# Kernel optimization log

Measured on AMD Instinct MI355X. Metric: run time of the kernel, lower is better.

## Reference

```python
import jax, jax.numpy as jnp
import numpy as np

N_FFT = 1024
N_STAGES = 3
N_SUB = N_FFT >> N_STAGES      # 128-point base IDFT
N_CHUNKS = 1 << N_STAGES       # 8 chunks after partial bit-reversal


def _mod_seq(order):
    mset = [0]
    for o in range(order):
        step = 2 ** o
        mset = [v for x in mset for v in (x, x + step)]
    return mset


def _perm_matrix(N, order):
    m = np.zeros((N, N), dtype=np.float32)
    base = 2 ** order
    k = 0
    for p in _mod_seq(order):
        for j in range(N // base):
            m[j * base + p, k] = 1.0
            k += 1
    return m


PERM = jnp.asarray(_perm_matrix(N_FFT, N_STAGES))
_idft = np.fft.ifft(np.eye(N_SUB))
IDFT_R = jnp.asarray(_idft.real.astype(np.float32))
IDFT_I = jnp.asarray(_idft.imag.astype(np.float32))


def _twiddle(n_fft_stage):
    w = np.exp(2j * np.pi / n_fft_stage) ** np.arange(n_fft_stage // 2)  # inverse sign
    return (jnp.asarray(w.real.astype(np.float32)),
            jnp.asarray(w.imag.astype(np.float32)))


TWIDDLES = []
_stage_size = N_FFT // 2 ** (N_STAGES - 1)
for _ in range(N_STAGES):
    TWIDDLES.append(_twiddle(_stage_size))
    _stage_size *= 2


def _idft_apply(re, im):
    yr = re @ IDFT_R.T - im @ IDFT_I.T
    yi = re @ IDFT_I.T + im @ IDFT_R.T
    return yr, yi


def _ifft_forward(re, im):
    # partial bit-reversal permutation then chunk
    re_p = jnp.split(re @ PERM, N_CHUNKS, axis=-1)
    im_p = jnp.split(im @ PERM, N_CHUNKS, axis=-1)
    ev_r, ev_i, od_r, od_i = [], [], [], []
    for j in range(N_CHUNKS // 2):
        er, ei = _idft_apply(re_p[2 * j], im_p[2 * j])
        o_r, o_i = _idft_apply(re_p[2 * j + 1], im_p[2 * j + 1])
        ev_r.append(er); ev_i.append(ei); od_r.append(o_r); od_i.append(o_i)
    # butterfly twiddle stages
    for tr, ti in TWIDDLES:
        ner, nei, nor, noi = [], [], [], []
        for i in range(len(ev_r)):
            todd_r = tr * od_r[i] - ti * od_i[i]
            todd_i = tr * od_i[i] + ti * od_r[i]
            real = jnp.concatenate([ev_r[i] + todd_r, ev_r[i] - todd_r], axis=-1)
            imag = jnp.concatenate([ev_i[i] + todd_i, ev_i[i] - todd_i], axis=-1)
            if i % 2 == 0:
                ner.append(real); nei.append(imag)
            else:
                nor.append(real); noi.append(imag)
        ev_r, ev_i, od_r, od_i = ner, nei, nor, noi
    scale = 1.0 / (1 << N_STAGES)  # IFFTNormalizer
    return ev_r[0] * scale, ev_i[0] * scale


def setup_inputs() -> dict:
    key = jax.random.key(0)
    k1, k2 = jax.random.split(key)
    re = jax.random.normal(k1, (8, 4096, N_FFT), dtype=jnp.float32)
    im = jax.random.normal(k2, (8, 4096, N_FFT), dtype=jnp.float32)
    return {"re": re, "im": im}


def reference(re, im):
    return _ifft_forward(re, im)
```

## Files before the change

kernel.cpp:

```cpp
#include <hip/hip_runtime.h>

#define NFFT 1024
#define TWO_PI 6.28318530717958647692f

__device__ __forceinline__ int SW(int a) {
    return a ^ ((((a >> 5) ^ (a >> 8)) & 7) << 2);
}

__device__ __forceinline__ void bfly4(float& r0, float& i0, float& r1, float& i1,
                                      float& r2, float& i2, float& r3, float& i3) {
    float d0r = r0 + r2, d0i = i0 + i2;
    float d1r = r0 - r2, d1i = i0 - i2;
    float d2r = r1 + r3, d2i = i1 + i3;
    float sr  = r1 - r3, si  = i1 - i3;
    r0 = d0r + d2r; i0 = d0i + d2i;
    r2 = d0r - d2r; i2 = d0i - d2i;
    r1 = d1r - si;  i1 = d1i + sr;
    r3 = d1r + si;  i3 = d1i - sr;
}

__device__ __forceinline__ void twmul(float& x, float& y, float c, float s) {
    float t = x * c - y * s;
    y = x * s + y * c;
    x = t;
}

__global__ __launch_bounds__(64, 4) void ifft1024_kernel(
        const float* __restrict__ re, const float* __restrict__ im,
        float* __restrict__ out, size_t imoff) {
    __shared__ __align__(16) float lds[2048];
    const int u = threadIdx.x;
    const size_t rowb = (size_t)blockIdx.x * NFFT;

    float vr[4][4], vi[4][4];

#pragma unroll
    for (int b = 0; b < 4; ++b)
#pragma unroll
        for (int a = 0; a < 4; ++a) {
            int idx = u + 64 * a + 256 * b;
            vr[a][b] = re[rowb + idx];
            vi[a][b] = im[rowb + idx];
        }

#pragma unroll
    for (int a = 0; a < 4; ++a) {
        bfly4(vr[a][0], vi[a][0], vr[a][1], vi[a][1],
              vr[a][2], vi[a][2], vr[a][3], vi[a][3]);
        float ang = (TWO_PI / 1024.f) * (float)(u + 64 * a);
        float s1, c1; __sincosf(ang, &s1, &c1);
        float c2 = c1 * c1 - s1 * s1, s2 = 2.f * c1 * s1;
        float c3 = c2 * c1 - s2 * s1, s3 = c2 * s1 + s2 * c1;
        twmul(vr[a][1], vi[a][1], c1, s1);
        twmul(vr[a][2], vi[a][2], c2, s2);
        twmul(vr[a][3], vi[a][3], c3, s3);
    }

    {
        float ang = (TWO_PI / 256.f) * (float)u;
        float s1, c1; __sincosf(ang, &s1, &c1);
        float c2 = c1 * c1 - s1 * s1, s2 = 2.f * c1 * s1;
        float c3 = c2 * c1 - s2 * s1, s3 = c2 * s1 + s2 * c1;
#pragma unroll
        for (int b = 0; b < 4; ++b) {
            bfly4(vr[0][b], vi[0][b], vr[1][b], vi[1][b],
                  vr[2][b], vi[2][b], vr[3][b], vi[3][b]);
            twmul(vr[1][b], vi[1][b], c1, s1);
            twmul(vr[2][b], vi[2][b], c2, s2);
            twmul(vr[3][b], vi[3][b], c3, s3);
        }
    }

#pragma unroll
    for (int b = 0; b < 4; ++b) {
        *(float4*)&lds[SW(16 * u + 4 * b)] =
            make_float4(vr[0][b], vr[1][b], vr[2][b], vr[3][b]);
        *(float4*)&lds[SW(16 * u + 4 * b + 1024)] =
            make_float4(vi[0][b], vi[1][b], vi[2][b], vi[3][b]);
    }
    __syncthreads();
    {
        int lo = (u >> 2) + 16 * (u & 3);
#pragma unroll
        for (int b = 0; b < 4; ++b)
#pragma unroll
            for (int a = 0; a < 4; ++a) {
                int q = lo + 64 * a + 256 * b;
                vr[a][b] = lds[SW(q)];
                vi[a][b] = lds[SW(q + 1024)];
            }
    }

    const int w = u & 3;
#pragma unroll
    for (int a = 0; a < 4; ++a) {
        bfly4(vr[a][0], vi[a][0], vr[a][1], vi[a][1],
              vr[a][2], vi[a][2], vr[a][3], vi[a][3]);
        float ang = (TWO_PI / 64.f) * (float)(w + 4 * a);
        float s1, c1; __sincosf(ang, &s1, &c1);
        float c2 = c1 * c1 - s1 * s1, s2 = 2.f * c1 * s1;
        float c3 = c2 * c1 - s2 * s1, s3 = c2 * s1 + s2 * c1;
        twmul(vr[a][1], vi[a][1], c1, s1);
        twmul(vr[a][2], vi[a][2], c2, s2);
        twmul(vr[a][3], vi[a][3], c3, s3);
    }

    {
        float ang = (TWO_PI / 16.f) * (float)w;
        float s1, c1; __sincosf(ang, &s1, &c1);
        float c2 = c1 * c1 - s1 * s1, s2 = 2.f * c1 * s1;
        float c3 = c2 * c1 - s2 * s1, s3 = c2 * s1 + s2 * c1;
#pragma unroll
        for (int b = 0; b < 4; ++b) {
            bfly4(vr[0][b], vi[0][b], vr[1][b], vi[1][b],
                  vr[2][b], vi[2][b], vr[3][b], vi[3][b]);
            twmul(vr[1][b], vi[1][b], c1, s1);
            twmul(vr[2][b], vi[2][b], c2, s2);
            twmul(vr[3][b], vi[3][b], c3, s3);
        }
    }
    __syncthreads();

#pragma unroll
    for (int a = 0; a < 4; ++a) {
        *(float4*)&lds[SW(16 * u + 4 * a)] =
            make_float4(vr[a][0], vr[a][1], vr[a][2], vr[a][3]);
        *(float4*)&lds[SW(16 * u + 4 * a + 1024)] =
            make_float4(vi[a][0], vi[a][1], vi[a][2], vi[a][3]);
    }
    __syncthreads();
    {
        int lo = (u & 3) + 64 * (u >> 2);
#pragma unroll
        for (int c = 0; c < 4; ++c)
#pragma unroll
            for (int e = 0; e < 4; ++e) {
                int q = lo + 4 * c + 16 * e;
                vr[c][e] = lds[SW(q)];
                vi[c][e] = lds[SW(q + 1024)];
            }
    }

#pragma unroll
    for (int c = 0; c < 4; ++c)
        bfly4(vr[c][0], vi[c][0], vr[c][1], vi[c][1],
              vr[c][2], vi[c][2], vr[c][3], vi[c][3]);

    const float sc = 1.f / 1024.f;
    const int nbase = 16 * (u & 3) + 4 * ((u >> 2) & 3) + (u >> 4);
#pragma unroll
    for (int e = 0; e < 4; ++e)
#pragma unroll
        for (int c = 0; c < 4; ++c) {
            int n = nbase + 64 * c + 256 * e;
            out[rowb + n]         = vr[c][e] * sc;
            out[imoff + rowb + n] = vi[c][e] * sc;
        }
}

extern "C" void kernel_launch(void* const* d_in, const int* in_sizes, int n_in,
                              void* d_out, int out_size, void* d_ws, size_t ws_size,
                              hipStream_t stream) {
    const float* re = (const float*)d_in[0];
    const float* im = (const float*)d_in[1];
    float* out = (float*)d_out;
    const int rows = in_sizes[0] / NFFT;
    const size_t im_off = (size_t)in_sizes[0];

    hipLaunchKernelGGL(ifft1024_kernel, dim3(rows), dim3(64), 0, stream,
                       re, im, out, im_off);
}
```

Before: 434.5 us.

## Pack four rows per block, one wavefront each, and restructure FFT data flow

Each 256-thread block now handles four 1024-point rows, one per wavefront, with a private LDS slice and only block-level fences in place of __syncthreads. Inputs are read as float4, twiddles come from one sincos plus rotation recurrences, and the last radix-16 stage uses constant twiddles after a float4 LDS read. A simpler XOR swizzle replaces the old one. This aims to cut per-block overhead, barrier cost and transcendental work, but it relies on wavefront-synchronous LDS behaviour and adds some twiddle rounding error from the recurrence.

Measured after the change: 433.2 us. Within noise of the previous version (-0.3%).

```diff
diff --git a/kernel.cpp b/kernel.cpp
--- a/kernel.cpp
+++ b/kernel.cpp
@@ -2,10 +2,6 @@
 
 #define NFFT 1024
 #define TWO_PI 6.28318530717958647692f
-
-__device__ __forceinline__ int SW(int a) {
-    return a ^ ((((a >> 5) ^ (a >> 8)) & 7) << 2);
-}
 
 __device__ __forceinline__ void bfly4(float& r0, float& i0, float& r1, float& i1,
                                       float& r2, float& i2, float& r3, float& i3) {
@@ -25,136 +21,164 @@
     x = t;
 }
 
-__global__ __launch_bounds__(64, 4) void ifft1024_kernel(
+__global__ __launch_bounds__(256, 4) void ifft1024_kernel(
         const float* __restrict__ re, const float* __restrict__ im,
         float* __restrict__ out, size_t imoff) {
-    __shared__ __align__(16) float lds[2048];
-    const int u = threadIdx.x;
-    const size_t rowb = (size_t)blockIdx.x * NFFT;
+    __shared__ __align__(16) float lds_all[8192];
+    const int tid = threadIdx.x;
+    const int u   = tid & 63;
+    const int wv  = tid >> 6;
+    float* lds = lds_all + (wv << 11);
+
+    const size_t row  = (size_t)blockIdx.x * 4 + wv;
+    const size_t rowb = row * NFFT;
 
     float vr[4][4], vi[4][4];
-
 #pragma unroll
-    for (int b = 0; b < 4; ++b)
-#pragma unroll
-        for (int a = 0; a < 4; ++a) {
-            int idx = u + 64 * a + 256 * b;
-            vr[a][b] = re[rowb + idx];
-            vi[a][b] = im[rowb + idx];
-        }
-
-#pragma unroll
-    for (int a = 0; a < 4; ++a) {
-        bfly4(vr[a][0], vi[a][0], vr[a][1], vi[a][1],
-              vr[a][2], vi[a][2], vr[a][3], vi[a][3]);
-        float ang = (TWO_PI / 1024.f) * (float)(u + 64 * a);
-        float s1, c1; __sincosf(ang, &s1, &c1);
-        float c2 = c1 * c1 - s1 * s1, s2 = 2.f * c1 * s1;
-        float c3 = c2 * c1 - s2 * s1, s3 = c2 * s1 + s2 * c1;
-        twmul(vr[a][1], vi[a][1], c1, s1);
-        twmul(vr[a][2], vi[a][2], c2, s2);
-        twmul(vr[a][3], vi[a][3], c3, s3);
+    for (int b = 0; b < 4; ++b) {
+        float4 r4 = *(const float4*)(re + rowb + 4 * u + 256 * b);
+        float4 i4 = *(const float4*)(im + rowb + 4 * u + 256 * b);
+        vr[0][b] = r4.x; vr[1][b] = r4.y; vr[2][b] = r4.z; vr[3][b] = r4.w;
+        vi[0][b] = i4.x; vi[1][b] = i4.y; vi[2][b] = i4.z; vi[3][b] = i4.w;
     }
 
     {
-        float ang = (TWO_PI / 256.f) * (float)u;
-        float s1, c1; __sincosf(ang, &s1, &c1);
-        float c2 = c1 * c1 - s1 * s1, s2 = 2.f * c1 * s1;
-        float c3 = c2 * c1 - s2 * s1, s3 = c2 * s1 + s2 * c1;
+        float c1, s1;
+        __sincosf((TWO_PI / 256.f) * (float)u, &s1, &c1);
+        const float CS = 0.9999811752826011f;
+        const float SN = 0.0061358846491544753f;
 #pragma unroll
-        for (int b = 0; b < 4; ++b) {
-            bfly4(vr[0][b], vi[0][b], vr[1][b], vi[1][b],
-                  vr[2][b], vi[2][b], vr[3][b], vi[3][b]);
-            twmul(vr[1][b], vi[1][b], c1, s1);
-            twmul(vr[2][b], vi[2][b], c2, s2);
-            twmul(vr[3][b], vi[3][b], c3, s3);
+        for (int k = 0; k < 4; ++k) {
+            bfly4(vr[k][0], vi[k][0], vr[k][1], vi[k][1],
+                  vr[k][2], vi[k][2], vr[k][3], vi[k][3]);
+            float c2 = c1 * c1 - s1 * s1, s2 = 2.f * c1 * s1;
+            float c3 = c2 * c1 - s2 * s1, s3 = c2 * s1 + s2 * c1;
+            twmul(vr[k][1], vi[k][1], c1, s1);
+            twmul(vr[k][2], vi[k][2], c2, s2);
+            twmul(vr[k][3], vi[k][3], c3, s3);
+            float nc = c1 * CS - s1 * SN, ns = c1 * SN + s1 * CS;
+            c1 = nc; s1 = ns;
         }
     }
 
 #pragma unroll
     for (int b = 0; b < 4; ++b) {
-        *(float4*)&lds[SW(16 * u + 4 * b)] =
-            make_float4(vr[0][b], vr[1][b], vr[2][b], vr[3][b]);
-        *(float4*)&lds[SW(16 * u + 4 * b + 1024)] =
-            make_float4(vi[0][b], vi[1][b], vi[2][b], vi[3][b]);
+        int q = (4 * u + 256 * b) ^ ((b & 1) << 4);
+        *(float4*)&lds[q]        = make_float4(vr[0][b], vr[1][b], vr[2][b], vr[3][b]);
+        *(float4*)&lds[q + 1024] = make_float4(vi[0][b], vi[1][b], vi[2][b], vi[3][b]);
     }
-    __syncthreads();
+    __threadfence_block();
+
+    const int j = u & 15, h = u >> 4;
+    const int flip = (h & 1) << 4;
+    float wr[4][4], wi[4][4];
     {
-        int lo = (u >> 2) + 16 * (u & 3);
+        const int rb = j + 256 * h;
 #pragma unroll
-        for (int b = 0; b < 4; ++b)
+        for (int a = 0; a < 4; ++a)
 #pragma unroll
-            for (int a = 0; a < 4; ++a) {
-                int q = lo + 64 * a + 256 * b;
-                vr[a][b] = lds[SW(q)];
-                vi[a][b] = lds[SW(q + 1024)];
+            for (int c = 0; c < 4; ++c) {
+                int q = rb + ((16 * a) ^ flip) + 64 * c;
+                wr[a][c] = lds[q];
+                wi[a][c] = lds[q + 1024];
             }
     }
 
-    const int w = u & 3;
+    {
+        float cA, sA;
+        __sincosf((TWO_PI / 256.f) * (float)j, &sA, &cA);
+        const float CS8 = 0.9238795325112867f;
+        const float SN8 = 0.3826834323650898f;
 #pragma unroll
-    for (int a = 0; a < 4; ++a) {
-        bfly4(vr[a][0], vi[a][0], vr[a][1], vi[a][1],
-              vr[a][2], vi[a][2], vr[a][3], vi[a][3]);
-        float ang = (TWO_PI / 64.f) * (float)(w + 4 * a);
-        float s1, c1; __sincosf(ang, &s1, &c1);
-        float c2 = c1 * c1 - s1 * s1, s2 = 2.f * c1 * s1;
-        float c3 = c2 * c1 - s2 * s1, s3 = c2 * s1 + s2 * c1;
-        twmul(vr[a][1], vi[a][1], c1, s1);
-        twmul(vr[a][2], vi[a][2], c2, s2);
-        twmul(vr[a][3], vi[a][3], c3, s3);
+        for (int a = 0; a < 4; ++a) {
+            bfly4(wr[a][0], wi[a][0], wr[a][1], wi[a][1],
+                  wr[a][2], wi[a][2], wr[a][3], wi[a][3]);
+            float c2 = cA * cA - sA * sA, s2 = 2.f * cA * sA;
+            float c3 = c2 * cA - s2 * sA, s3 = c2 * sA + s2 * cA;
+            twmul(wr[a][1], wi[a][1], cA, sA);
+            twmul(wr[a][2], wi[a][2], c2, s2);
+            twmul(wr[a][3], wi[a][3], c3, s3);
+            float nc = cA * CS8 - sA * SN8, ns = cA * SN8 + sA * CS8;
+            cA = nc; sA = ns;
+        }
     }
 
     {
-        float ang = (TWO_PI / 16.f) * (float)w;
-        float s1, c1; __sincosf(ang, &s1, &c1);
-        float c2 = c1 * c1 - s1 * s1, s2 = 2.f * c1 * s1;
-        float c3 = c2 * c1 - s2 * s1, s3 = c2 * s1 + s2 * c1;
+        float cB, sB;
+        __sincosf((TWO_PI / 64.f) * (float)j, &sB, &cB);
+        float cB2 = cB * cB - sB * sB, sB2 = 2.f * cB * sB;
+        float cB3 = cB2 * cB - sB2 * sB, sB3 = cB2 * sB + sB2 * cB;
 #pragma unroll
-        for (int b = 0; b < 4; ++b) {
-            bfly4(vr[0][b], vi[0][b], vr[1][b], vi[1][b],
-                  vr[2][b], vi[2][b], vr[3][b], vi[3][b]);
-            twmul(vr[1][b], vi[1][b], c1, s1);
-            twmul(vr[2][b], vi[2][b], c2, s2);
-            twmul(vr[3][b], vi[3][b], c3, s3);
+        for (int c = 0; c < 4; ++c) {
+            bfly4(wr[0][c], wi[0][c], wr[1][c], wi[1][c],
+                  wr[2][c], wi[2][c], wr[3][c], wi[3][c]);
+            twmul(wr[1][c], wi[1][c], cB, sB);
+            twmul(wr[2][c], wi[2][c], cB2, sB2);
+            twmul(wr[3][c], wi[3][c], cB3, sB3);
         }
     }
-    __syncthreads();
 
+    __threadfence_block();
+    {
+        const int rb = j + 256 * h;
 #pragma unroll
-    for (int a = 0; a < 4; ++a) {
-        *(float4*)&lds[SW(16 * u + 4 * a)] =
-            make_float4(vr[a][0], vr[a][1], vr[a][2], vr[a][3]);
-        *(float4*)&lds[SW(16 * u + 4 * a + 1024)] =
-            make_float4(vi[a][0], vi[a][1], vi[a][2], vi[a][3]);
+        for (int a = 0; a < 4; ++a)
+#pragma unroll
+            for (int c = 0; c < 4; ++c) {
+                int q = rb + ((16 * a) ^ flip) + 64 * c;
+                lds[q]        = wr[a][c];
+                lds[q + 1024] = wi[a][c];
+            }
     }
-    __syncthreads();
+    __threadfence_block();
+
+    float yr[4][4], yi[4][4];
     {
-        int lo = (u & 3) + 64 * (u >> 2);
+        const int rb = (16 * u) ^ flip;
 #pragma unroll
-        for (int c = 0; c < 4; ++c)
-#pragma unroll
-            for (int e = 0; e < 4; ++e) {
-                int q = lo + 4 * c + 16 * e;
-                vr[c][e] = lds[SW(q)];
-                vi[c][e] = lds[SW(q + 1024)];
-            }
+        for (int e = 0; e < 4; ++e) {
+            float4 r4 = *(const float4*)&lds[rb + 4 * e];
+            float4 i4 = *(const float4*)&lds[rb + 4 * e + 1024];
+            yr[e][0] = r4.x; yr[e][1] = r4.y; yr[e][2] = r4.z; yr[e][3] = r4.w;
+            yi[e][0] = i4.x; yi[e][1] = i4.y; yi[e][2] = i4.z; yi[e][3] = i4.w;
+        }
     }
 
 #pragma unroll
-    for (int c = 0; c < 4; ++c)
-        bfly4(vr[c][0], vi[c][0], vr[c][1], vi[c][1],
-              vr[c][2], vi[c][2], vr[c][3], vi[c][3]);
+    for (int f = 0; f < 4; ++f)
+        bfly4(yr[0][f], yi[0][f], yr[1][f], yi[1][f],
+              yr[2][f], yi[2][f], yr[3][f], yi[3][f]);
+    {
+        const float C1 = 0.9238795325112867f,  S1 = 0.3826834323650898f;
+        const float C2 = 0.7071067811865476f,  S2 = 0.7071067811865476f;
+        const float C3 = 0.3826834323650898f,  S3 = 0.9238795325112867f;
+        const float C6 = -0.7071067811865476f, S6 = 0.7071067811865476f;
+        const float C9 = -0.9238795325112867f, S9 = -0.3826834323650898f;
+        twmul(yr[1][1], yi[1][1], C1, S1);
+        twmul(yr[2][1], yi[2][1], C2, S2);
+        twmul(yr[3][1], yi[3][1], C3, S3);
+        twmul(yr[1][2], yi[1][2], C2, S2);
+        twmul(yr[2][2], yi[2][2], 0.f, 1.f);
+        twmul(yr[3][2], yi[3][2], C6, S6);
+        twmul(yr[1][3], yi[1][3], C3, S3);
+        twmul(yr[2][3], yi[2][3], C6, S6);
+        twmul(yr[3][3], yi[3][3], C9, S9);
+    }
+
+#pragma unroll
+    for (int e = 0; e < 4; ++e)
+        bfly4(yr[e][0], yi[e][0], yr[e][1], yi[e][1],
+              yr[e][2], yi[e][2], yr[e][3], yi[e][3]);
 
     const float sc = 1.f / 1024.f;
-    const int nbase = 16 * (u & 3) + 4 * ((u >> 2) & 3) + (u >> 4);
+    const int nb = 16 * (u & 3) + 4 * ((u >> 2) & 3) + (u >> 4);
 #pragma unroll
-    for (int e = 0; e < 4; ++e)
+    for (int f = 0; f < 4; ++f)
 #pragma unroll
-        for (int c = 0; c < 4; ++c) {
-            int n = nbase + 64 * c + 256 * e;
-            out[rowb + n]         = vr[c][e] * sc;
-            out[imoff + rowb + n] = vi[c][e] * sc;
+        for (int e = 0; e < 4; ++e) {
+            int n = nb + 64 * e + 256 * f;
+            out[rowb + n]         = yr[e][f] * sc;
+            out[imoff + rowb + n] = yi[e][f] * sc;
         }
 }
 
@@ -167,6 +191,6 @@
     const int rows = in_sizes[0] / NFFT;
     const size_t im_off = (size_t)in_sizes[0];
 
-    hipLaunchKernelGGL(ifft1024_kernel, dim3(rows), dim3(64), 0, stream,
+    hipLaunchKernelGGL(ifft1024_kernel, dim3(rows / 4), dim3(256), 0, stream,
                        re, im, out, im_off);
 }
```
